# Performance work log

Hardware: AMD Instinct MI355X
Metric: run time of the kernel (lower is better)

## Reference

```python
import jax, jax.numpy as jnp
import numpy as np

K_NEIGHBORS = 3  # self.K in DSVDD


def setup_inputs() -> dict:
    key = jax.random.key(0)
    k1, k2 = jax.random.split(key)
    B, N, C = 16, 3136, 112   # batch, h*w patches, descriptor channels
    M = 3136                  # memory-bank size
    phi_p = jax.random.normal(k1, (B, N, C), dtype=jnp.float32)
    C_bank = jax.random.normal(k2, (C, M), dtype=jnp.float32)
    return {"phi_p": phi_p, "C_bank": C_bank, "h": 56}


def reference(phi_p, C_bank, h):
    # squared distances via ||phi||^2 + ||c||^2 - 2 phi.c  -> (B, N, M)
    features = jnp.sum(phi_p * phi_p, axis=2, keepdims=True)        # (B, N, 1)
    centers = jnp.sum(C_bank * C_bank, axis=0, keepdims=True)       # (1, M)
    f_c = 2.0 * jnp.einsum('bnc,cm->bnm', phi_p, C_bank)            # (B, N, M)
    dist = jnp.sqrt(features + centers - f_c)                        # (B, N, M)
    # K smallest distances (ascending, like torch.topk(largest=False))
    neg_topk, _ = jax.lax.top_k(-dist, K_NEIGHBORS)                  # (B, N, K)
    dist_k = -neg_topk
    # softmin over K, take weight of the nearest neighbor times its distance
    softmin0 = jax.nn.softmax(-dist_k, axis=-1)[:, :, 0]             # (B, N)
    score = softmin0 * dist_k[:, :, 0]                               # (B, N)
    B, N = score.shape
    w = N // h
    return score.reshape(B, 1, h, w)  # b c h w with c=1
```

## Files before the change

kernel.cpp:

```cpp
#include <hip/hip_runtime.h>
#include <stdint.h>


typedef short s16x8 __attribute__((ext_vector_type(8)));
typedef float fx4 __attribute__((ext_vector_type(4)));

#define M_TOT 3136
#define CC 112
#define N_MTILES 25

__device__ __forceinline__ unsigned short f2bf(float x) {
  unsigned u = __float_as_uint(x);
  u += 0x7fffu + ((u >> 16) & 1u);
  return (unsigned short)(u >> 16);
}

__device__ __forceinline__ void async16(const void* g, void* l) {
  __builtin_amdgcn_global_load_lds(
      (const __attribute__((address_space(1))) unsigned int*)g,
      (__attribute__((address_space(3))) unsigned int*)l, 16, 0, 0);
}

#define INSERT3(T0, T1, T2, V)                                  \
  do {                                                          \
    const float _a0 = (T0), _a1 = (T1), _v = (V);               \
    (T0) = fmaxf(_a0, _v);                                      \
    (T1) = __builtin_amdgcn_fmed3f(_a0, _a1, _v);               \
    (T2) = __builtin_amdgcn_fmed3f(_a1, (T2), _v);              \
  } while (0)

__global__ __launch_bounds__(256) void dsvdd_prep(const float* __restrict__ Cb,
                                                  unsigned char* __restrict__ CTg) {
  const int i = threadIdx.x & 63;
  const int q = threadIdx.x >> 6;
  const int m = blockIdx.x * 64 + i;
  const bool valid = (m < M_TOT);
  __shared__ float part[4][64];
  float ss = 0.f;
  const int b0 = q * 4;
  const int nb = (q == 3) ? 2 : 4;
  for (int jb = 0; jb < nb; ++jb) {
    const int b = b0 + jb;
    float v[8];
#pragma unroll
    for (int j = 0; j < 8; ++j) {
      v[j] = valid ? Cb[(size_t)(b * 8 + j) * M_TOT + m] : 0.f;
      ss += v[j] * v[j];
    }
    uint4 pk;
    pk.x = (unsigned)f2bf(v[0]) | ((unsigned)f2bf(v[1]) << 16);
    pk.y = (unsigned)f2bf(v[2]) | ((unsigned)f2bf(v[3]) << 16);
    pk.z = (unsigned)f2bf(v[4]) | ((unsigned)f2bf(v[5]) << 16);
    pk.w = (unsigned)f2bf(v[6]) | ((unsigned)f2bf(v[7]) << 16);
    *(uint4*)(CTg + (size_t)m * 256 + ((b ^ (m & 7)) * 16)) = pk;
  }
  part[q][i] = ss;
  __syncthreads();
  if (q == 0) {
    const float c2 = part[0][i] + part[1][i] + part[2][i] + part[3][i];
    const float slot = valid ? (-0.125f * c2) : -2500.0f;
    const unsigned sb = f2bf(slot);
    const unsigned ww = sb | (sb << 16);
    uint4 blk;
    blk.x = ww; blk.y = ww; blk.z = 0u; blk.w = 0u;
    *(uint4*)(CTg + (size_t)m * 256 + ((14 ^ (m & 7)) * 16)) = blk;
    uint4 zz;
    zz.x = zz.y = zz.z = zz.w = 0u;
    *(uint4*)(CTg + (size_t)m * 256 + ((15 ^ (m & 7)) * 16)) = zz;
  }
}

__global__ __launch_bounds__(256, 2) void dsvdd_main(const float* __restrict__ phi,
                                                     const unsigned char* __restrict__ CTg,
                                                     float* __restrict__ out) {
  __shared__ __align__(16) unsigned char phi_lds[128 * 256];
  __shared__ __align__(16) unsigned char ct_lds[128 * 256];
  __shared__ float feat_lds[128];
  __shared__ float merge_lds[128][8];

  const int t = threadIdx.x;
  const int lane = t & 63;
  const int w = t >> 6;
  const int wm = w & 1;
  const int wp = w >> 1;
  const long rowBase = (long)blockIdx.x * 128;

  {
    const int r = t >> 1;
    const int half = t & 1;
    const float* src = phi + (rowBase + r) * CC + half * 56;
    float ss = 0.f;
#pragma unroll
    for (int j = 0; j < 7; ++j) {
      const float4 v0 = *(const float4*)(src + j * 8);
      const float4 v1 = *(const float4*)(src + j * 8 + 4);
      ss += v0.x * v0.x + v0.y * v0.y + v0.z * v0.z + v0.w * v0.w;
      ss += v1.x * v1.x + v1.y * v1.y + v1.z * v1.z + v1.w * v1.w;
      uint4 pk;
      pk.x = (unsigned)f2bf(v0.x) | ((unsigned)f2bf(v0.y) << 16);
      pk.y = (unsigned)f2bf(v0.z) | ((unsigned)f2bf(v0.w) << 16);
      pk.z = (unsigned)f2bf(v1.x) | ((unsigned)f2bf(v1.y) << 16);
      pk.w = (unsigned)f2bf(v1.z) | ((unsigned)f2bf(v1.w) << 16);
      const int b = half * 7 + j;
      *(uint4*)(phi_lds + r * 256 + ((b ^ (r & 7)) * 16)) = pk;
    }
    {
      const int b = 14 + half;
      uint4 pk;
      if (half == 0) {
        pk.x = 0x3f803f80u; pk.y = 0x3f803f80u; pk.z = 0u; pk.w = 0u;
      } else {
        pk.x = pk.y = pk.z = pk.w = 0u;
      }
      *(uint4*)(phi_lds + r * 256 + ((b ^ (r & 7)) * 16)) = pk;
    }
    ss += __shfl_xor(ss, 1);
    if (half == 0) feat_lds[r] = ss;
  }

  float t0[4], t1[4], t2[4];
#pragma unroll
  for (int pf = 0; pf < 4; ++pf) t0[pf] = t1[pf] = t2[pf] = -3.0e38f;

  {
    const unsigned char* g = CTg + (size_t)w * 8192 + lane * 16;
    unsigned char* l = ct_lds + w * 8192;
#pragma unroll
    for (int ii = 0; ii < 8; ++ii) async16(g + ii * 1024, l + ii * 1024);
  }
  __syncthreads();

  const int cq = lane & 15;
  const int kq = lane >> 4;
  const int sw = lane & 7;

  for (int mt = 0; mt < N_MTILES; ++mt) {
    fx4 acc[4][4];
    const fx4 zz = {0.f, 0.f, 0.f, 0.f};
#pragma unroll
    for (int ks = 0; ks < 4; ++ks) {
      s16x8 af[4], bg[4];
      const int pb = (ks * 4 + kq) ^ sw;
#pragma unroll
      for (int mf = 0; mf < 4; ++mf)
        af[mf] = *(const s16x8*)(ct_lds + (wm * 64 + mf * 16 + cq) * 256 + pb * 16);
#pragma unroll
      for (int pf = 0; pf < 4; ++pf)
        bg[pf] = *(const s16x8*)(phi_lds + (wp * 64 + pf * 16 + cq) * 256 + pb * 16);
#pragma unroll
      for (int mf = 0; mf < 4; ++mf)
#pragma unroll
        for (int pf = 0; pf < 4; ++pf)
          acc[mf][pf] = __builtin_amdgcn_mfma_f32_16x16x32_bf16(
              af[mf], bg[pf], (ks == 0) ? zz : acc[mf][pf], 0, 0, 0);
    }
    __syncthreads();

    if (mt + 1 < N_MTILES) {
      const unsigned char* g = CTg + (size_t)(mt + 1) * 32768 + (size_t)w * 8192 + lane * 16;
      unsigned char* l = ct_lds + w * 8192;
#pragma unroll
      for (int ii = 0; ii < 8; ++ii) async16(g + ii * 1024, l + ii * 1024);
    }

#pragma unroll
    for (int mf = 0; mf < 4; ++mf)
#pragma unroll
      for (int pf = 0; pf < 4; ++pf)
#pragma unroll
        for (int rg = 0; rg < 4; ++rg)
          INSERT3(t0[pf], t1[pf], t2[pf], acc[mf][pf][rg]);

    if (mt + 1 < N_MTILES) __syncthreads();
  }

#pragma unroll
  for (int pf = 0; pf < 4; ++pf) {
#pragma unroll
    for (int off = 16; off < 64; off <<= 1) {
      const float b0 = __shfl_xor(t0[pf], off);
      const float b1 = __shfl_xor(t1[pf], off);
      const float b2 = __shfl_xor(t2[pf], off);
      INSERT3(t0[pf], t1[pf], t2[pf], b0);
      INSERT3(t0[pf], t1[pf], t2[pf], b1);
      INSERT3(t0[pf], t1[pf], t2[pf], b2);
    }
  }
  if (kq == 0) {
#pragma unroll
    for (int pf = 0; pf < 4; ++pf) {
      const int row = wp * 64 + pf * 16 + cq;
      merge_lds[row][wm * 4 + 0] = t0[pf];
      merge_lds[row][wm * 4 + 1] = t1[pf];
      merge_lds[row][wm * 4 + 2] = t2[pf];
    }
  }
  __syncthreads();

  if (t < 128) {
    float s0 = merge_lds[t][0], s1 = merge_lds[t][1], s2 = merge_lds[t][2];
    INSERT3(s0, s1, s2, merge_lds[t][4]);
    INSERT3(s0, s1, s2, merge_lds[t][5]);
    INSERT3(s0, s1, s2, merge_lds[t][6]);
    const float feat = feat_lds[t];
    const float d0 = sqrtf(fmaxf(feat - 2.f * s0, 0.f));
    const float d1 = sqrtf(fmaxf(feat - 2.f * s1, 0.f));
    const float d2 = sqrtf(fmaxf(feat - 2.f * s2, 0.f));
    const float w0 = 1.0f / (1.0f + __expf(d0 - d1) + __expf(d0 - d2));
    out[rowBase + t] = w0 * d0;
  }
}

extern "C" void kernel_launch(void* const* d_in, const int* in_sizes, int n_in,
                              void* d_out, int out_size, void* d_ws, size_t ws_size,
                              hipStream_t stream) {
  (void)in_sizes; (void)n_in; (void)out_size; (void)ws_size;
  const float* phi = (const float*)d_in[0];
  const float* Cb = (const float*)d_in[1];
  float* out = (float*)d_out;
  unsigned char* CTg = (unsigned char*)d_ws;
  dsvdd_prep<<<50, 256, 0, stream>>>(Cb, CTg);
  dsvdd_main<<<392, 256, 0, stream>>>(phi, CTg, out);
}
```

Baseline: 66.00 us.

## Keep phi fragments in registers and double-buffer bank tiles in LDS

Each wave now loads its full 128-row phi operand into registers once and covers 32 bank columns against all 128 rows, where before waves were split 2x2. The bank tile is double-buffered in LDS, which removes one barrier per tile and overlaps the next async load with the MFMA work. The aim is fewer LDS reads per MFMA and fewer synchronisations. The cost is much higher register use (32 B-fragments plus 8 top-3 triplets), which may cause spills or lower occupancy, and an enlarged merge step across four waves.

```diff
diff --git a/kernel.cpp b/kernel.cpp
--- a/kernel.cpp
+++ b/kernel.cpp
@@ -73,17 +73,26 @@
 __global__ __launch_bounds__(256, 2) void dsvdd_main(const float* __restrict__ phi,
                                                      const unsigned char* __restrict__ CTg,
                                                      float* __restrict__ out) {
-  __shared__ __align__(16) unsigned char phi_lds[128 * 256];
-  __shared__ __align__(16) unsigned char ct_lds[128 * 256];
-  __shared__ float feat_lds[128];
-  __shared__ float merge_lds[128][8];
+  __shared__ __align__(16) unsigned char smem[66048];
+  unsigned char* const buf0 = smem;
+  unsigned char* const buf1 = smem + 32768;
+  float* const feat_lds = (float*)(smem + 65536);
+  float(*const merge_lds)[17] = (float(*)[17])smem;
 
   const int t = threadIdx.x;
   const int lane = t & 63;
   const int w = t >> 6;
-  const int wm = w & 1;
-  const int wp = w >> 1;
   const long rowBase = (long)blockIdx.x * 128;
+  const int cq = lane & 15;
+  const int kq = lane >> 4;
+  const int sw = lane & 7;
+
+  {
+    const unsigned char* g = CTg + (size_t)w * 8192 + lane * 16;
+    unsigned char* l = buf0 + w * 8192;
+#pragma unroll
+    for (int ii = 0; ii < 8; ++ii) async16(g + ii * 1024, l + ii * 1024);
+  }
 
   {
     const int r = t >> 1;
@@ -102,7 +111,7 @@
       pk.z = (unsigned)f2bf(v1.x) | ((unsigned)f2bf(v1.y) << 16);
       pk.w = (unsigned)f2bf(v1.z) | ((unsigned)f2bf(v1.w) << 16);
       const int b = half * 7 + j;
-      *(uint4*)(phi_lds + r * 256 + ((b ^ (r & 7)) * 16)) = pk;
+      *(uint4*)(buf1 + r * 256 + ((b ^ (r & 7)) * 16)) = pk;
     }
     {
       const int b = 14 + half;
@@ -112,70 +121,61 @@
       } else {
         pk.x = pk.y = pk.z = pk.w = 0u;
       }
-      *(uint4*)(phi_lds + r * 256 + ((b ^ (r & 7)) * 16)) = pk;
+      *(uint4*)(buf1 + r * 256 + ((b ^ (r & 7)) * 16)) = pk;
     }
     ss += __shfl_xor(ss, 1);
     if (half == 0) feat_lds[r] = ss;
   }
-
-  float t0[4], t1[4], t2[4];
-#pragma unroll
-  for (int pf = 0; pf < 4; ++pf) t0[pf] = t1[pf] = t2[pf] = -3.0e38f;
-
-  {
-    const unsigned char* g = CTg + (size_t)w * 8192 + lane * 16;
-    unsigned char* l = ct_lds + w * 8192;
-#pragma unroll
-    for (int ii = 0; ii < 8; ++ii) async16(g + ii * 1024, l + ii * 1024);
-  }
-  __syncthreads();
-
-  const int cq = lane & 15;
-  const int kq = lane >> 4;
-  const int sw = lane & 7;
-
+  __syncthreads();
+
+  s16x8 bg[4][8];
+#pragma unroll
+  for (int ks = 0; ks < 4; ++ks)
+#pragma unroll
+    for (int pf = 0; pf < 8; ++pf)
+      bg[ks][pf] = *(const s16x8*)(buf1 + (pf * 16 + cq) * 256 + (((ks * 4 + kq) ^ sw) * 16));
+  __syncthreads();
+
+  float t0[8], t1[8], t2[8];
+#pragma unroll
+  for (int pf = 0; pf < 8; ++pf) t0[pf] = t1[pf] = t2[pf] = -3.0e38f;
+
+  const fx4 zz = {0.f, 0.f, 0.f, 0.f};
   for (int mt = 0; mt < N_MTILES; ++mt) {
-    fx4 acc[4][4];
-    const fx4 zz = {0.f, 0.f, 0.f, 0.f};
-#pragma unroll
-    for (int ks = 0; ks < 4; ++ks) {
-      s16x8 af[4], bg[4];
-      const int pb = (ks * 4 + kq) ^ sw;
-#pragma unroll
-      for (int mf = 0; mf < 4; ++mf)
-        af[mf] = *(const s16x8*)(ct_lds + (wm * 64 + mf * 16 + cq) * 256 + pb * 16);
-#pragma unroll
-      for (int pf = 0; pf < 4; ++pf)
-        bg[pf] = *(const s16x8*)(phi_lds + (wp * 64 + pf * 16 + cq) * 256 + pb * 16);
-#pragma unroll
-      for (int mf = 0; mf < 4; ++mf)
-#pragma unroll
-        for (int pf = 0; pf < 4; ++pf)
-          acc[mf][pf] = __builtin_amdgcn_mfma_f32_16x16x32_bf16(
-              af[mf], bg[pf], (ks == 0) ? zz : acc[mf][pf], 0, 0, 0);
-    }
-    __syncthreads();
+    const unsigned char* rd = smem + ((mt & 1) ? 32768 : 0);
+    unsigned char* wr = smem + ((mt & 1) ? 0 : 32768);
 
     if (mt + 1 < N_MTILES) {
       const unsigned char* g = CTg + (size_t)(mt + 1) * 32768 + (size_t)w * 8192 + lane * 16;
-      unsigned char* l = ct_lds + w * 8192;
+      unsigned char* l = wr + w * 8192;
 #pragma unroll
       for (int ii = 0; ii < 8; ++ii) async16(g + ii * 1024, l + ii * 1024);
     }
 
 #pragma unroll
-    for (int mf = 0; mf < 4; ++mf)
-#pragma unroll
-      for (int pf = 0; pf < 4; ++pf)
+    for (int mf = 0; mf < 2; ++mf) {
+      s16x8 af[4];
+#pragma unroll
+      for (int ks = 0; ks < 4; ++ks)
+        af[ks] = *(const s16x8*)(rd + (w * 32 + mf * 16 + cq) * 256 + (((ks * 4 + kq) ^ sw) * 16));
+      fx4 acc[8];
+#pragma unroll
+      for (int ks = 0; ks < 4; ++ks)
+#pragma unroll
+        for (int pf = 0; pf < 8; ++pf)
+          acc[pf] = __builtin_amdgcn_mfma_f32_16x16x32_bf16(
+              af[ks], bg[ks][pf], (ks == 0) ? zz : acc[pf], 0, 0, 0);
+#pragma unroll
+      for (int pf = 0; pf < 8; ++pf)
 #pragma unroll
         for (int rg = 0; rg < 4; ++rg)
-          INSERT3(t0[pf], t1[pf], t2[pf], acc[mf][pf][rg]);
-
-    if (mt + 1 < N_MTILES) __syncthreads();
-  }
-
-#pragma unroll
-  for (int pf = 0; pf < 4; ++pf) {
+          INSERT3(t0[pf], t1[pf], t2[pf], acc[pf][rg]);
+    }
+    __syncthreads();
+  }
+
+#pragma unroll
+  for (int pf = 0; pf < 8; ++pf) {
 #pragma unroll
     for (int off = 16; off < 64; off <<= 1) {
       const float b0 = __shfl_xor(t0[pf], off);
@@ -188,20 +188,23 @@
   }
   if (kq == 0) {
 #pragma unroll
-    for (int pf = 0; pf < 4; ++pf) {
-      const int row = wp * 64 + pf * 16 + cq;
-      merge_lds[row][wm * 4 + 0] = t0[pf];
-      merge_lds[row][wm * 4 + 1] = t1[pf];
-      merge_lds[row][wm * 4 + 2] = t2[pf];
+    for (int pf = 0; pf < 8; ++pf) {
+      const int row = pf * 16 + cq;
+      merge_lds[row][w * 4 + 0] = t0[pf];
+      merge_lds[row][w * 4 + 1] = t1[pf];
+      merge_lds[row][w * 4 + 2] = t2[pf];
     }
   }
   __syncthreads();
 
   if (t < 128) {
     float s0 = merge_lds[t][0], s1 = merge_lds[t][1], s2 = merge_lds[t][2];
-    INSERT3(s0, s1, s2, merge_lds[t][4]);
-    INSERT3(s0, s1, s2, merge_lds[t][5]);
-    INSERT3(s0, s1, s2, merge_lds[t][6]);
+#pragma unroll
+    for (int ww2 = 1; ww2 < 4; ++ww2) {
+      INSERT3(s0, s1, s2, merge_lds[t][ww2 * 4 + 0]);
+      INSERT3(s0, s1, s2, merge_lds[t][ww2 * 4 + 1]);
+      INSERT3(s0, s1, s2, merge_lds[t][ww2 * 4 + 2]);
+    }
     const float feat = feat_lds[t];
     const float d0 = sqrtf(fmaxf(feat - 2.f * s0, 0.f));
     const float d1 = sqrtf(fmaxf(feat - 2.f * s1, 0.f));
```

Measured after the change: 65.74 us. About the same (-0.4%).

## Hold phi fragments in registers and stream bank fragments directly from global

Applied to the files above, without the earlier changes.

The main kernel now runs 512 threads in two groups of four waves. Each wave keeps its 64-row phi B-fragments resident in registers for the whole kernel. The centre-bank A-fragments are loaded straight from global/L2 into registers with double buffering, replacing the LDS staging and its per-tile syncthreads. The prep kernel drops the XOR swizzle because the bank no longer goes through LDS. The merge buffer reuses the phi LDS region and now merges four partial top-3 sets. This removes LDS traffic and barriers but raises register pressure and depends on L2 bandwidth for repeated bank reads.

```diff
diff --git a/kernel.cpp b/kernel.cpp
--- a/kernel.cpp
+++ b/kernel.cpp
@@ -13,12 +13,6 @@
   unsigned u = __float_as_uint(x);
   u += 0x7fffu + ((u >> 16) & 1u);
   return (unsigned short)(u >> 16);
-}
-
-__device__ __forceinline__ void async16(const void* g, void* l) {
-  __builtin_amdgcn_global_load_lds(
-      (const __attribute__((address_space(1))) unsigned int*)g,
-      (__attribute__((address_space(3))) unsigned int*)l, 16, 0, 0);
 }
 
 #define INSERT3(T0, T1, T2, V)                                  \
@@ -52,7 +46,7 @@
     pk.y = (unsigned)f2bf(v[2]) | ((unsigned)f2bf(v[3]) << 16);
     pk.z = (unsigned)f2bf(v[4]) | ((unsigned)f2bf(v[5]) << 16);
     pk.w = (unsigned)f2bf(v[6]) | ((unsigned)f2bf(v[7]) << 16);
-    *(uint4*)(CTg + (size_t)m * 256 + ((b ^ (m & 7)) * 16)) = pk;
+    *(uint4*)(CTg + (size_t)m * 256 + b * 16) = pk;
   }
   part[q][i] = ss;
   __syncthreads();
@@ -63,29 +57,31 @@
     const unsigned ww = sb | (sb << 16);
     uint4 blk;
     blk.x = ww; blk.y = ww; blk.z = 0u; blk.w = 0u;
-    *(uint4*)(CTg + (size_t)m * 256 + ((14 ^ (m & 7)) * 16)) = blk;
+    *(uint4*)(CTg + (size_t)m * 256 + 14 * 16) = blk;
     uint4 zz;
     zz.x = zz.y = zz.z = zz.w = 0u;
-    *(uint4*)(CTg + (size_t)m * 256 + ((15 ^ (m & 7)) * 16)) = zz;
-  }
-}
-
-__global__ __launch_bounds__(256, 2) void dsvdd_main(const float* __restrict__ phi,
+    *(uint4*)(CTg + (size_t)m * 256 + 15 * 16) = zz;
+  }
+}
+
+__global__ __launch_bounds__(512, 2) void dsvdd_main(const float* __restrict__ phi,
                                                      const unsigned char* __restrict__ CTg,
                                                      float* __restrict__ out) {
   __shared__ __align__(16) unsigned char phi_lds[128 * 256];
-  __shared__ __align__(16) unsigned char ct_lds[128 * 256];
   __shared__ float feat_lds[128];
-  __shared__ float merge_lds[128][8];
+  float(*const merge_lds)[17] = (float(*)[17])phi_lds;
 
   const int t = threadIdx.x;
   const int lane = t & 63;
   const int w = t >> 6;
-  const int wm = w & 1;
-  const int wp = w >> 1;
+  const int g = w >> 2;
+  const int ms = w & 3;
+  const int cq = lane & 15;
+  const int kq = lane >> 4;
+  const int sw = lane & 7;
   const long rowBase = (long)blockIdx.x * 128;
 
-  {
+  if (t < 256) {
     const int r = t >> 1;
     const int half = t & 1;
     const float* src = phi + (rowBase + r) * CC + half * 56;
@@ -117,62 +113,60 @@
     ss += __shfl_xor(ss, 1);
     if (half == 0) feat_lds[r] = ss;
   }
+  __syncthreads();
+
+  s16x8 bg[4][4];
+#pragma unroll
+  for (int ks = 0; ks < 4; ++ks)
+#pragma unroll
+    for (int pf = 0; pf < 4; ++pf)
+      bg[ks][pf] = *(const s16x8*)(phi_lds + (g * 64 + pf * 16 + cq) * 256 +
+                                   (((ks * 4 + kq) ^ sw) * 16));
 
   float t0[4], t1[4], t2[4];
 #pragma unroll
   for (int pf = 0; pf < 4; ++pf) t0[pf] = t1[pf] = t2[pf] = -3.0e38f;
 
-  {
-    const unsigned char* g = CTg + (size_t)w * 8192 + lane * 16;
-    unsigned char* l = ct_lds + w * 8192;
-#pragma unroll
-    for (int ii = 0; ii < 8; ++ii) async16(g + ii * 1024, l + ii * 1024);
-  }
-  __syncthreads();
-
-  const int cq = lane & 15;
-  const int kq = lane >> 4;
-  const int sw = lane & 7;
-
-  for (int mt = 0; mt < N_MTILES; ++mt) {
-    fx4 acc[4][4];
-    const fx4 zz = {0.f, 0.f, 0.f, 0.f};
-#pragma unroll
-    for (int ks = 0; ks < 4; ++ks) {
-      s16x8 af[4], bg[4];
-      const int pb = (ks * 4 + kq) ^ sw;
-#pragma unroll
-      for (int mf = 0; mf < 4; ++mf)
-        af[mf] = *(const s16x8*)(ct_lds + (wm * 64 + mf * 16 + cq) * 256 + pb * 16);
-#pragma unroll
-      for (int pf = 0; pf < 4; ++pf)
-        bg[pf] = *(const s16x8*)(phi_lds + (wp * 64 + pf * 16 + cq) * 256 + pb * 16);
-#pragma unroll
-      for (int mf = 0; mf < 4; ++mf)
-#pragma unroll
-        for (int pf = 0; pf < 4; ++pf)
-          acc[mf][pf] = __builtin_amdgcn_mfma_f32_16x16x32_bf16(
-              af[mf], bg[pf], (ks == 0) ? zz : acc[mf][pf], 0, 0, 0);
-    }
-    __syncthreads();
-
-    if (mt + 1 < N_MTILES) {
-      const unsigned char* g = CTg + (size_t)(mt + 1) * 32768 + (size_t)w * 8192 + lane * 16;
-      unsigned char* l = ct_lds + w * 8192;
-#pragma unroll
-      for (int ii = 0; ii < 8; ++ii) async16(g + ii * 1024, l + ii * 1024);
-    }
-
-#pragma unroll
-    for (int mf = 0; mf < 4; ++mf)
-#pragma unroll
-      for (int pf = 0; pf < 4; ++pf)
-#pragma unroll
-        for (int rg = 0; rg < 4; ++rg)
-          INSERT3(t0[pf], t1[pf], t2[pf], acc[mf][pf][rg]);
-
-    if (mt + 1 < N_MTILES) __syncthreads();
-  }
+  const unsigned char* ap = CTg + (size_t)(ms * 32 + cq) * 256 + kq * 16;
+
+  s16x8 afA[8], afB[8];
+
+#define LOADAF(DST, MT)                                                       \
+  do {                                                                        \
+    const unsigned char* _p = ap + (size_t)(MT)*32768;                        \
+    _Pragma("unroll") for (int mf = 0; mf < 2; ++mf)                          \
+        _Pragma("unroll") for (int ks = 0; ks < 4; ++ks)                      \
+            DST[mf * 4 + ks] = *(const s16x8*)(_p + mf * 4096 + ks * 64);     \
+  } while (0)
+
+#define COMPUTE(SRC)                                                          \
+  do {                                                                        \
+    const fx4 _zz = {0.f, 0.f, 0.f, 0.f};                                     \
+    _Pragma("unroll") for (int mf = 0; mf < 2; ++mf) {                        \
+      fx4 acc[4];                                                             \
+      _Pragma("unroll") for (int ks = 0; ks < 4; ++ks)                        \
+          _Pragma("unroll") for (int pf = 0; pf < 4; ++pf)                    \
+              acc[pf] = __builtin_amdgcn_mfma_f32_16x16x32_bf16(              \
+                  SRC[mf * 4 + ks], bg[ks][pf], (ks == 0) ? _zz : acc[pf],    \
+                  0, 0, 0);                                                   \
+      _Pragma("unroll") for (int pf = 0; pf < 4; ++pf)                        \
+          _Pragma("unroll") for (int rg = 0; rg < 4; ++rg)                    \
+              INSERT3(t0[pf], t1[pf], t2[pf], acc[pf][rg]);                   \
+    }                                                                         \
+  } while (0)
+
+  LOADAF(afA, 0);
+  for (int mtp = 0; mtp < 12; ++mtp) {
+    LOADAF(afB, 2 * mtp + 1);
+    COMPUTE(afA);
+    __builtin_amdgcn_s_barrier();
+    LOADAF(afA, 2 * mtp + 2);
+    COMPUTE(afB);
+  }
+  COMPUTE(afA);
+
+#undef LOADAF
+#undef COMPUTE
 
 #pragma unroll
   for (int pf = 0; pf < 4; ++pf) {
@@ -186,22 +180,26 @@
       INSERT3(t0[pf], t1[pf], t2[pf], b2);
     }
   }
+  __syncthreads();
   if (kq == 0) {
 #pragma unroll
     for (int pf = 0; pf < 4; ++pf) {
-      const int row = wp * 64 + pf * 16 + cq;
-      merge_lds[row][wm * 4 + 0] = t0[pf];
-      merge_lds[row][wm * 4 + 1] = t1[pf];
-      merge_lds[row][wm * 4 + 2] = t2[pf];
+      const int row = g * 64 + pf * 16 + cq;
+      merge_lds[row][ms * 4 + 0] = t0[pf];
+      merge_lds[row][ms * 4 + 1] = t1[pf];
+      merge_lds[row][ms * 4 + 2] = t2[pf];
     }
   }
   __syncthreads();
 
   if (t < 128) {
     float s0 = merge_lds[t][0], s1 = merge_lds[t][1], s2 = merge_lds[t][2];
-    INSERT3(s0, s1, s2, merge_lds[t][4]);
-    INSERT3(s0, s1, s2, merge_lds[t][5]);
-    INSERT3(s0, s1, s2, merge_lds[t][6]);
+#pragma unroll
+    for (int ww2 = 1; ww2 < 4; ++ww2) {
+      INSERT3(s0, s1, s2, merge_lds[t][ww2 * 4 + 0]);
+      INSERT3(s0, s1, s2, merge_lds[t][ww2 * 4 + 1]);
+      INSERT3(s0, s1, s2, merge_lds[t][ww2 * 4 + 2]);
+    }
     const float feat = feat_lds[t];
     const float d0 = sqrtf(fmaxf(feat - 2.f * s0, 0.f));
     const float d1 = sqrtf(fmaxf(feat - 2.f * s1, 0.f));
@@ -220,5 +218,5 @@
   float* out = (float*)d_out;
   unsigned char* CTg = (unsigned char*)d_ws;
   dsvdd_prep<<<50, 256, 0, stream>>>(Cb, CTg);
-  dsvdd_main<<<392, 256, 0, stream>>>(phi, CTg, out);
-}
+  dsvdd_main<<<392, 512, 0, stream>>>(phi, CTg, out);
+}
```

New measurement: 113.2 us. +71.5%, slower.

## Split memory-bank tiles across grid (split-K over M) with register-held phi and two-stage top-3 merge

Applied to the files above, without the earlier changes.

The main kernel is split into a stage that distributes the memory-bank tiles across a second grid dimension (up to 5 chunks). Phi fragments are kept in registers instead of LDS, the bank tiles are double-buffered in smaller 16KB halves with a 16-way XOR swizzle, and occupancy is raised to 4 blocks per CU. Per-chunk top-3 partials go to workspace and a second small kernel merges them and computes the softmin score. This targets the low block count (392 blocks) and the serialized tile loop, in exchange for an extra launch, recomputed phi conversion per chunk, and workspace traffic.

```diff
diff --git a/kernel.cpp b/kernel.cpp
--- a/kernel.cpp
+++ b/kernel.cpp
@@ -7,7 +7,8 @@
 
 #define M_TOT 3136
 #define CC 112
-#define N_MTILES 25
+#define NROWS 50176
+#define N_TILES_TOT 50
 
 __device__ __forceinline__ unsigned short f2bf(float x) {
   unsigned u = __float_as_uint(x);
@@ -52,7 +53,7 @@
     pk.y = (unsigned)f2bf(v[2]) | ((unsigned)f2bf(v[3]) << 16);
     pk.z = (unsigned)f2bf(v[4]) | ((unsigned)f2bf(v[5]) << 16);
     pk.w = (unsigned)f2bf(v[6]) | ((unsigned)f2bf(v[7]) << 16);
-    *(uint4*)(CTg + (size_t)m * 256 + ((b ^ (m & 7)) * 16)) = pk;
+    *(uint4*)(CTg + (size_t)m * 256 + ((b ^ (m & 15)) * 16)) = pk;
   }
   part[q][i] = ss;
   __syncthreads();
@@ -63,115 +64,113 @@
     const unsigned ww = sb | (sb << 16);
     uint4 blk;
     blk.x = ww; blk.y = ww; blk.z = 0u; blk.w = 0u;
-    *(uint4*)(CTg + (size_t)m * 256 + ((14 ^ (m & 7)) * 16)) = blk;
+    *(uint4*)(CTg + (size_t)m * 256 + ((14 ^ (m & 15)) * 16)) = blk;
     uint4 zz;
     zz.x = zz.y = zz.z = zz.w = 0u;
-    *(uint4*)(CTg + (size_t)m * 256 + ((15 ^ (m & 7)) * 16)) = zz;
-  }
-}
-
-__global__ __launch_bounds__(256, 2) void dsvdd_main(const float* __restrict__ phi,
-                                                     const unsigned char* __restrict__ CTg,
-                                                     float* __restrict__ out) {
-  __shared__ __align__(16) unsigned char phi_lds[128 * 256];
-  __shared__ __align__(16) unsigned char ct_lds[128 * 256];
-  __shared__ float feat_lds[128];
-  __shared__ float merge_lds[128][8];
+    *(uint4*)(CTg + (size_t)m * 256 + ((15 ^ (m & 15)) * 16)) = zz;
+  }
+}
+
+__global__ __launch_bounds__(256, 4) void dsvdd_stage1(const float* __restrict__ phi,
+                                                       const unsigned char* __restrict__ CTg,
+                                                       float* __restrict__ part,
+                                                       float* __restrict__ featg, int nT) {
+  __shared__ __align__(16) unsigned char lds[32768];
+  unsigned char* const buf0 = lds;
+  unsigned char* const buf1 = lds + 16384;
 
   const int t = threadIdx.x;
   const int lane = t & 63;
   const int w = t >> 6;
-  const int wm = w & 1;
-  const int wp = w >> 1;
-  const long rowBase = (long)blockIdx.x * 128;
-
-  {
-    const int r = t >> 1;
-    const int half = t & 1;
-    const float* src = phi + (rowBase + r) * CC + half * 56;
-    float ss = 0.f;
-#pragma unroll
-    for (int j = 0; j < 7; ++j) {
-      const float4 v0 = *(const float4*)(src + j * 8);
-      const float4 v1 = *(const float4*)(src + j * 8 + 4);
-      ss += v0.x * v0.x + v0.y * v0.y + v0.z * v0.z + v0.w * v0.w;
-      ss += v1.x * v1.x + v1.y * v1.y + v1.z * v1.z + v1.w * v1.w;
-      uint4 pk;
-      pk.x = (unsigned)f2bf(v0.x) | ((unsigned)f2bf(v0.y) << 16);
-      pk.y = (unsigned)f2bf(v0.z) | ((unsigned)f2bf(v0.w) << 16);
-      pk.z = (unsigned)f2bf(v1.x) | ((unsigned)f2bf(v1.y) << 16);
-      pk.w = (unsigned)f2bf(v1.z) | ((unsigned)f2bf(v1.w) << 16);
-      const int b = half * 7 + j;
-      *(uint4*)(phi_lds + r * 256 + ((b ^ (r & 7)) * 16)) = pk;
-    }
-    {
-      const int b = 14 + half;
-      uint4 pk;
-      if (half == 0) {
-        pk.x = 0x3f803f80u; pk.y = 0x3f803f80u; pk.z = 0u; pk.w = 0u;
-      } else {
-        pk.x = pk.y = pk.z = pk.w = 0u;
-      }
-      *(uint4*)(phi_lds + r * 256 + ((b ^ (r & 7)) * 16)) = pk;
-    }
-    ss += __shfl_xor(ss, 1);
-    if (half == 0) feat_lds[r] = ss;
-  }
-
-  float t0[4], t1[4], t2[4];
-#pragma unroll
-  for (int pf = 0; pf < 4; ++pf) t0[pf] = t1[pf] = t2[pf] = -3.0e38f;
-
-  {
-    const unsigned char* g = CTg + (size_t)w * 8192 + lane * 16;
-    unsigned char* l = ct_lds + w * 8192;
-#pragma unroll
-    for (int ii = 0; ii < 8; ++ii) async16(g + ii * 1024, l + ii * 1024);
-  }
-  __syncthreads();
-
+  const int g = w >> 1;
+  const int h = w & 1;
   const int cq = lane & 15;
   const int kq = lane >> 4;
-  const int sw = lane & 7;
-
-  for (int mt = 0; mt < N_MTILES; ++mt) {
-    fx4 acc[4][4];
-    const fx4 zz = {0.f, 0.f, 0.f, 0.f};
+  const int c = blockIdx.y;
+  const int tile0 = c * nT;
+  const long rowBase = (long)blockIdx.x * 128;
+
+  {
+    const unsigned char* gsrc = CTg + (size_t)tile0 * 16384 + w * 1024 + lane * 16;
+    unsigned char* ldst = buf0 + w * 1024;
+#pragma unroll
+    for (int r = 0; r < 4; ++r) async16(gsrc + r * 4096, ldst + r * 4096);
+  }
+
+  s16x8 bg[4][4];
+  float ssr[4];
+#pragma unroll
+  for (int pf = 0; pf < 4; ++pf) {
+    ssr[pf] = 0.f;
+    const float* rp = phi + (size_t)(rowBase + g * 64 + pf * 16 + cq) * CC;
 #pragma unroll
     for (int ks = 0; ks < 4; ++ks) {
-      s16x8 af[4], bg[4];
-      const int pb = (ks * 4 + kq) ^ sw;
-#pragma unroll
-      for (int mf = 0; mf < 4; ++mf)
-        af[mf] = *(const s16x8*)(ct_lds + (wm * 64 + mf * 16 + cq) * 256 + pb * 16);
+      const int k0 = ks * 32 + kq * 8;
+      s16x8 v;
+      if (k0 <= 104) {
+        const float4 a = *(const float4*)(rp + k0);
+        const float4 b = *(const float4*)(rp + k0 + 4);
+        ssr[pf] += a.x * a.x + a.y * a.y + a.z * a.z + a.w * a.w;
+        ssr[pf] += b.x * b.x + b.y * b.y + b.z * b.z + b.w * b.w;
+        v[0] = (short)f2bf(a.x); v[1] = (short)f2bf(a.y);
+        v[2] = (short)f2bf(a.z); v[3] = (short)f2bf(a.w);
+        v[4] = (short)f2bf(b.x); v[5] = (short)f2bf(b.y);
+        v[6] = (short)f2bf(b.z); v[7] = (short)f2bf(b.w);
+      } else if (k0 == 112) {
+        v[0] = v[1] = v[2] = v[3] = (short)0x3f80;
+        v[4] = v[5] = v[6] = v[7] = 0;
+      } else {
+        v = (s16x8)0;
+      }
+      bg[ks][pf] = v;
+    }
+    ssr[pf] += __shfl_xor(ssr[pf], 16);
+    ssr[pf] += __shfl_xor(ssr[pf], 32);
+  }
+  if (c == 0 && kq == 0) {
+#pragma unroll
+    for (int pf = 0; pf < 4; ++pf)
+      featg[rowBase + g * 64 + pf * 16 + cq] = ssr[pf];
+  }
+
+  float t0[4], t1[4], t2[4];
+#pragma unroll
+  for (int pf = 0; pf < 4; ++pf) t0[pf] = t1[pf] = t2[pf] = -3.0e38f;
+
+  __syncthreads();
+
+  for (int tt = 0; tt < nT; ++tt) {
+    const unsigned char* rd = (tt & 1) ? buf1 : buf0;
+    unsigned char* wr = (tt & 1) ? buf0 : buf1;
+    if (tt + 1 < nT) {
+      const unsigned char* gsrc =
+          CTg + (size_t)(tile0 + tt + 1) * 16384 + w * 1024 + lane * 16;
+      unsigned char* ldst = wr + w * 1024;
+#pragma unroll
+      for (int r = 0; r < 4; ++r) async16(gsrc + r * 4096, ldst + r * 4096);
+    }
+#pragma unroll
+    for (int mf = 0; mf < 2; ++mf) {
+      const unsigned char* abase = rd + (h * 32 + mf * 16 + cq) * 256;
+      s16x8 af[4];
+#pragma unroll
+      for (int ks = 0; ks < 4; ++ks)
+        af[ks] = *(const s16x8*)(abase + (((ks * 4 + kq) ^ cq) * 16));
+      fx4 acc[4];
+      const fx4 zz = {0.f, 0.f, 0.f, 0.f};
+#pragma unroll
+      for (int ks = 0; ks < 4; ++ks)
+#pragma unroll
+        for (int pf = 0; pf < 4; ++pf)
+          acc[pf] = __builtin_amdgcn_mfma_f32_16x16x32_bf16(
+              af[ks], bg[ks][pf], (ks == 0) ? zz : acc[pf], 0, 0, 0);
 #pragma unroll
       for (int pf = 0; pf < 4; ++pf)
-        bg[pf] = *(const s16x8*)(phi_lds + (wp * 64 + pf * 16 + cq) * 256 + pb * 16);
-#pragma unroll
-      for (int mf = 0; mf < 4; ++mf)
-#pragma unroll
-        for (int pf = 0; pf < 4; ++pf)
-          acc[mf][pf] = __builtin_amdgcn_mfma_f32_16x16x32_bf16(
-              af[mf], bg[pf], (ks == 0) ? zz : acc[mf][pf], 0, 0, 0);
+#pragma unroll
+        for (int rg = 0; rg < 4; ++rg)
+          INSERT3(t0[pf], t1[pf], t2[pf], acc[pf][rg]);
     }
     __syncthreads();
-
-    if (mt + 1 < N_MTILES) {
-      const unsigned char* g = CTg + (size_t)(mt + 1) * 32768 + (size_t)w * 8192 + lane * 16;
-      unsigned char* l = ct_lds + w * 8192;
-#pragma unroll
-      for (int ii = 0; ii < 8; ++ii) async16(g + ii * 1024, l + ii * 1024);
-    }
-
-#pragma unroll
-    for (int mf = 0; mf < 4; ++mf)
-#pragma unroll
-      for (int pf = 0; pf < 4; ++pf)
-#pragma unroll
-        for (int rg = 0; rg < 4; ++rg)
-          INSERT3(t0[pf], t1[pf], t2[pf], acc[mf][pf][rg]);
-
-    if (mt + 1 < N_MTILES) __syncthreads();
   }
 
 #pragma unroll
@@ -186,39 +185,63 @@
       INSERT3(t0[pf], t1[pf], t2[pf], b2);
     }
   }
+  float(*const mg)[8] = (float(*)[8])lds;
   if (kq == 0) {
 #pragma unroll
     for (int pf = 0; pf < 4; ++pf) {
-      const int row = wp * 64 + pf * 16 + cq;
-      merge_lds[row][wm * 4 + 0] = t0[pf];
-      merge_lds[row][wm * 4 + 1] = t1[pf];
-      merge_lds[row][wm * 4 + 2] = t2[pf];
+      const int row = g * 64 + pf * 16 + cq;
+      mg[row][h * 3 + 0] = t0[pf];
+      mg[row][h * 3 + 1] = t1[pf];
+      mg[row][h * 3 + 2] = t2[pf];
     }
   }
   __syncthreads();
-
   if (t < 128) {
-    float s0 = merge_lds[t][0], s1 = merge_lds[t][1], s2 = merge_lds[t][2];
-    INSERT3(s0, s1, s2, merge_lds[t][4]);
-    INSERT3(s0, s1, s2, merge_lds[t][5]);
-    INSERT3(s0, s1, s2, merge_lds[t][6]);
-    const float feat = feat_lds[t];
-    const float d0 = sqrtf(fmaxf(feat - 2.f * s0, 0.f));
-    const float d1 = sqrtf(fmaxf(feat - 2.f * s1, 0.f));
-    const float d2 = sqrtf(fmaxf(feat - 2.f * s2, 0.f));
-    const float w0 = 1.0f / (1.0f + __expf(d0 - d1) + __expf(d0 - d2));
-    out[rowBase + t] = w0 * d0;
-  }
+    float s0 = mg[t][0], s1 = mg[t][1], s2 = mg[t][2];
+    INSERT3(s0, s1, s2, mg[t][3]);
+    INSERT3(s0, s1, s2, mg[t][4]);
+    INSERT3(s0, s1, s2, mg[t][5]);
+    float* dst = part + ((size_t)c * NROWS + rowBase + t) * 3;
+    dst[0] = s0; dst[1] = s1; dst[2] = s2;
+  }
+}
+
+__global__ __launch_bounds__(256) void dsvdd_stage2(const float* __restrict__ part,
+                                                    const float* __restrict__ featg,
+                                                    float* __restrict__ out, int S) {
+  const int row = blockIdx.x * 256 + threadIdx.x;
+  if (row >= NROWS) return;
+  float s0 = -3.0e38f, s1 = -3.0e38f, s2 = -3.0e38f;
+  for (int c = 0; c < S; ++c) {
+    const float* p = part + ((size_t)c * NROWS + row) * 3;
+    INSERT3(s0, s1, s2, p[0]);
+    INSERT3(s0, s1, s2, p[1]);
+    INSERT3(s0, s1, s2, p[2]);
+  }
+  const float feat = featg[row];
+  const float d0 = sqrtf(fmaxf(feat - 2.f * s0, 0.f));
+  const float d1 = sqrtf(fmaxf(feat - 2.f * s1, 0.f));
+  const float d2 = sqrtf(fmaxf(feat - 2.f * s2, 0.f));
+  const float w0 = 1.0f / (1.0f + __expf(d0 - d1) + __expf(d0 - d2));
+  out[row] = w0 * d0;
 }
 
 extern "C" void kernel_launch(void* const* d_in, const int* in_sizes, int n_in,
                               void* d_out, int out_size, void* d_ws, size_t ws_size,
                               hipStream_t stream) {
-  (void)in_sizes; (void)n_in; (void)out_size; (void)ws_size;
+  (void)in_sizes; (void)n_in; (void)out_size;
   const float* phi = (const float*)d_in[0];
   const float* Cb = (const float*)d_in[1];
   float* out = (float*)d_out;
   unsigned char* CTg = (unsigned char*)d_ws;
+  float* featg = (float*)((unsigned char*)d_ws + 819200);
+  float* partp = (float*)((unsigned char*)d_ws + 819200 + 200704);
+  const size_t base = 819200 + 200704;
+  int S = 1;
+  if (ws_size >= base + (size_t)5 * NROWS * 12) S = 5;
+  else if (ws_size >= base + (size_t)2 * NROWS * 12) S = 2;
+  const int nT = N_TILES_TOT / S;
   dsvdd_prep<<<50, 256, 0, stream>>>(Cb, CTg);
-  dsvdd_main<<<392, 256, 0, stream>>>(phi, CTg, out);
-}
+  dsvdd_stage1<<<dim3(392, S), 256, 0, stream>>>(phi, CTg, partp, featg, nT);
+  dsvdd_stage2<<<196, 256, 0, stream>>>(partp, featg, out, S);
+}
```

Result: slower. 79.23 us (+20.0%).
